# Performance work log

Measured on AMD Instinct MI355X. Metric: run time of the kernel, lower is better.

## Reference

```python
import jax, jax.numpy as jnp
import numpy as np

L, H, C, HS, V, BS = 4, 8, 512, 64, 32000, 2048  # layers, heads, n_embd, head_size, vocab, block_size
B, T = 2, 2048


def _ln(x, g, b, eps=1e-5):
    m = jnp.mean(x, axis=-1, keepdims=True)
    v = jnp.var(x, axis=-1, keepdims=True)
    return (x - m) * jax.lax.rsqrt(v + eps) * g + b


def setup_inputs() -> dict:
    key = jax.random.key(0)
    ks = jax.random.split(key, 12)
    s = 0.02
    f = jnp.float32
    return {
        "idx": jax.random.randint(ks[0], (B, T), 0, V),
        "tok_emb": jax.random.normal(ks[1], (V, C), f) * s,
        "pos_emb": jax.random.normal(ks[2], (BS, C), f) * s,
        "ln1_g": jnp.ones((L, C), f), "ln1_b": jnp.zeros((L, C), f),
        "wq": jax.random.normal(ks[3], (L, H, C, HS), f) * s,
        "wk": jax.random.normal(ks[4], (L, H, C, HS), f) * s,
        "wv": jax.random.normal(ks[5], (L, H, C, HS), f) * s,
        "proj_w": jax.random.normal(ks[6], (L, C, C), f) * s,
        "proj_b": jnp.zeros((L, C), f),
        "ln2_g": jnp.ones((L, C), f), "ln2_b": jnp.zeros((L, C), f),
        "ff_w1": jax.random.normal(ks[7], (L, C, 4 * C), f) * s,
        "ff_b1": jnp.zeros((L, 4 * C), f),
        "ff_w2": jax.random.normal(ks[8], (L, 4 * C, C), f) * s,
        "ff_b2": jnp.zeros((L, C), f),
        "ffln_g": jnp.ones((L, C), f), "ffln_b": jnp.zeros((L, C), f),
        "lm_w": jax.random.normal(ks[9], (C, V), f) * s,
        "lm_b": jnp.zeros((V,), f),
    }


def reference(idx, tok_emb, pos_emb, ln1_g, ln1_b, wq, wk, wv, proj_w, proj_b,
              ln2_g, ln2_b, ff_w1, ff_b1, ff_w2, ff_b2, ffln_g, ffln_b, lm_w, lm_b):
    Tn = idx.shape[1]
    x = tok_emb[idx] + pos_emb[:Tn]  # [B,T,C]
    causal = jnp.tril(jnp.ones((Tn, Tn), bool))
    for l in range(L):
        h = _ln(x, ln1_g[l], ln1_b[l])
        q = jnp.einsum('btc,hcd->bhtd', h, wq[l])
        k = jnp.einsum('btc,hcd->bhtd', h, wk[l])
        v = jnp.einsum('btc,hcd->bhtd', h, wv[l])
        # NOTE: original module does NOT scale by 1/sqrt(head_size)
        wei = jnp.einsum('bhtd,bhsd->bhts', q, k)
        wei = jnp.where(causal, wei, -jnp.inf)
        wei = jax.nn.softmax(wei, axis=-1)
        att = jnp.einsum('bhts,bhsd->bhtd', wei, v)  # [B,H,T,HS]
        att = att.transpose(0, 2, 1, 3).reshape(x.shape[0], Tn, C)
        x = x + att @ proj_w[l].T + proj_b[l]
        h2 = _ln(x, ln2_g[l], ln2_b[l])
        ff = jax.nn.relu(h2 @ ff_w1[l] + ff_b1[l]) @ ff_w2[l] + ff_b2[l]
        ff = _ln(ff, ffln_g[l], ffln_b[l])  # FeedForward has trailing LayerNorm
        x = x + ff
    logits = x @ lm_w + lm_b  # [B,T,V]
    return logits
```

## Files before the change

kernel.cpp:

```cpp
#include <hip/hip_runtime.h>
#include <math.h>

#define NLAYER 4
#define NH     8
#define CDIM   512
#define HS     64
#define VOCAB  32000
#define BB     2
#define TT     2048
#define MROWS  (BB*TT)
#define QKVW   (3*CDIM)
#define NHEADS (BB*NH)

typedef __attribute__((ext_vector_type(8))) short bf16x8;
typedef __attribute__((ext_vector_type(4))) float f32x4;

__device__ __forceinline__ unsigned short f2bf(float f) {
    unsigned int u = __float_as_uint(f);
    u += 0x7FFF + ((u >> 16) & 1);
    return (unsigned short)(u >> 16);
}

#define GLOAD16(g, l) __builtin_amdgcn_global_load_lds( \
    (const __attribute__((address_space(1))) void*)(g), \
    (__attribute__((address_space(3))) void*)(l), 16, 0, 0)

template<int FLAGS, bool OUTBF>
__global__ __launch_bounds__(256) void mfma_gemm(
    const unsigned short* __restrict__ A, int lda,
    const unsigned short* __restrict__ Bt, int ldb,
    const float* __restrict__ bias,
    void* __restrict__ Cout, int ldc,
    const float* __restrict__ resid,
    int K)
{
    __shared__ unsigned short As[128*64];
    __shared__ unsigned short Bs[128*64];
    const int tid = threadIdx.x;
    const int w = tid >> 6, l = tid & 63;
    const int wr = w >> 1, wc = w & 1;
    const long m0 = (long)blockIdx.y * 128;
    const long n0 = (long)blockIdx.x * 128;
    const int srow = l >> 3;
    const int scol = (l & 7) << 3;
    const unsigned short* Ab = A + m0*lda;
    const unsigned short* Bb = Bt + n0*ldb;
    const int fr = l & 15;
    const int fk = (l >> 4) << 3;

    f32x4 acc[4][4];
    #pragma unroll
    for (int m = 0; m < 4; m++)
        #pragma unroll
        for (int n = 0; n < 4; n++) acc[m][n] = (f32x4)0.0f;

    for (int k0 = 0; k0 < K; k0 += 64) {
        __syncthreads();
        #pragma unroll
        for (int i = 0; i < 4; i++) {
            int seg = w*4 + i;
            GLOAD16(Ab + (long)(seg*8 + srow)*lda + k0 + scol, As + seg*512);
            GLOAD16(Bb + (long)(seg*8 + srow)*ldb + k0 + scol, Bs + seg*512);
        }
        __syncthreads();
        #pragma unroll
        for (int kk = 0; kk < 2; kk++) {
            bf16x8 af[4], bf[4];
            #pragma unroll
            for (int m = 0; m < 4; m++)
                af[m] = *(const bf16x8*)&As[(wr*64 + m*16 + fr)*64 + kk*32 + fk];
            #pragma unroll
            for (int n = 0; n < 4; n++)
                bf[n] = *(const bf16x8*)&Bs[(wc*64 + n*16 + fr)*64 + kk*32 + fk];
            #pragma unroll
            for (int m = 0; m < 4; m++)
                #pragma unroll
                for (int n = 0; n < 4; n++)
                    acc[m][n] = __builtin_amdgcn_mfma_f32_16x16x32_bf16(
                        af[m], bf[n], acc[m][n], 0, 0, 0);
        }
    }

    const int rg = (l >> 4) << 2;
    #pragma unroll
    for (int n = 0; n < 4; n++) {
        long gn = n0 + wc*64 + n*16 + fr;
        float bv = (FLAGS & 1) ? bias[gn] : 0.f;
        #pragma unroll
        for (int m = 0; m < 4; m++) {
            #pragma unroll
            for (int r = 0; r < 4; r++) {
                long gm = m0 + wr*64 + m*16 + rg + r;
                float val = acc[m][n][r] + bv;
                if (FLAGS & 2) val = fmaxf(val, 0.f);
                if (FLAGS & 4) val += resid[gm*ldc + gn];
                if (OUTBF) ((unsigned short*)Cout)[gm*ldc + gn] = f2bf(val);
                else       ((float*)Cout)[gm*ldc + gn] = val;
            }
        }
    }
}

__global__ __launch_bounds__(256) void mfma_gemm_qkv(
    const unsigned short* __restrict__ A,
    const unsigned short* __restrict__ Bt,
    unsigned short* __restrict__ qh,
    unsigned short* __restrict__ kh,
    unsigned short* __restrict__ vt)
{
    __shared__ unsigned short As[128*64];
    __shared__ unsigned short Bs[128*64];
    const int tid = threadIdx.x;
    const int w = tid >> 6, l = tid & 63;
    const int wr = w >> 1, wc = w & 1;
    const long m0 = (long)blockIdx.y * 128;
    const long n0 = (long)blockIdx.x * 128;
    const int srow = l >> 3;
    const int scol = (l & 7) << 3;
    const unsigned short* Ab = A + m0*CDIM;
    const unsigned short* Bb = Bt + n0*CDIM;
    const int fr = l & 15;
    const int fk = (l >> 4) << 3;

    f32x4 acc[4][4];
    #pragma unroll
    for (int m = 0; m < 4; m++)
        #pragma unroll
        for (int n = 0; n < 4; n++) acc[m][n] = (f32x4)0.0f;

    for (int k0 = 0; k0 < CDIM; k0 += 64) {
        __syncthreads();
        #pragma unroll
        for (int i = 0; i < 4; i++) {
            int seg = w*4 + i;
            GLOAD16(Ab + (long)(seg*8 + srow)*CDIM + k0 + scol, As + seg*512);
            GLOAD16(Bb + (long)(seg*8 + srow)*CDIM + k0 + scol, Bs + seg*512);
        }
        __syncthreads();
        #pragma unroll
        for (int kk = 0; kk < 2; kk++) {
            bf16x8 af[4], bf[4];
            #pragma unroll
            for (int m = 0; m < 4; m++)
                af[m] = *(const bf16x8*)&As[(wr*64 + m*16 + fr)*64 + kk*32 + fk];
            #pragma unroll
            for (int n = 0; n < 4; n++)
                bf[n] = *(const bf16x8*)&Bs[(wc*64 + n*16 + fr)*64 + kk*32 + fk];
            #pragma unroll
            for (int m = 0; m < 4; m++)
                #pragma unroll
                for (int n = 0; n < 4; n++)
                    acc[m][n] = __builtin_amdgcn_mfma_f32_16x16x32_bf16(
                        af[m], bf[n], acc[m][n], 0, 0, 0);
        }
    }

    const int rg = (l >> 4) << 2;
    #pragma unroll
    for (int n = 0; n < 4; n++) {
        int gn = (int)(n0 + wc*64 + n*16 + fr);
        int which = gn >> 9, hh = (gn >> 6) & 7, d = gn & 63;
        #pragma unroll
        for (int m = 0; m < 4; m++) {
            #pragma unroll
            for (int r = 0; r < 4; r++) {
                int gm = (int)(m0 + wr*64 + m*16 + rg + r);
                int b = gm >> 11, t = gm & (TT-1);
                int head = b*NH + hh;
                unsigned short val = f2bf(acc[m][n][r]);
                if (which == 0)      qh[((long)head*TT + t)*HS + d] = val;
                else if (which == 1) kh[((long)head*TT + t)*HS + d] = val;
                else                 vt[((long)head*HS + d)*TT + t] = val;
            }
        }
    }
}

__global__ __launch_bounds__(256) void attn_part(
    const unsigned short* __restrict__ qh,
    const unsigned short* __restrict__ kh,
    const unsigned short* __restrict__ vt,
    float* __restrict__ oP, float* __restrict__ ml)
{
    __shared__ unsigned short Ks[2][64*64];
    __shared__ unsigned short Vts[2][64*64];
    __shared__ unsigned short Ps[4][32*72];
    const int tid = threadIdx.x;
    const int w = tid >> 6, l = tid & 63;
    const int fr = l & 15, g = l >> 4;
    const int head = blockIdx.y;
    const int sp = blockIdx.z;
    const int x = blockIdx.x;
    const int qt0 = x * 128;
    const int qw = qt0 + w*32;
    const unsigned short* Qb = qh + (long)head*TT*HS;
    const unsigned short* Kb = kh + (long)head*TT*HS;
    const unsigned short* Vb = vt + (long)head*HS*TT;

    bf16x8 aq[2][2];
    #pragma unroll
    for (int mt = 0; mt < 2; mt++)
        #pragma unroll
        for (int ks = 0; ks < 2; ks++)
            aq[mt][ks] = *(const bf16x8*)&Qb[(long)(qw + mt*16 + fr)*HS + ks*32 + g*8];

    f32x4 acc_o[2][4];
    float mrun[2][4], lsum[2][4];
    #pragma unroll
    for (int mt = 0; mt < 2; mt++) {
        #pragma unroll
        for (int r = 0; r < 4; r++) { mrun[mt][r] = -INFINITY; lsum[mt][r] = 0.f; }
        #pragma unroll
        for (int n = 0; n < 4; n++) acc_o[mt][n] = (f32x4)0.0f;
    }

    const int cbeg = sp * (x + 1);
    const int cend = cbeg + (x + 1);
    const int srow = l >> 3;
    const int scol = ((l & 7) ^ (srow & 7)) << 3;

    auto stage = [&](int c) {
        int buf = c & 1;
        int s0_ = c*64;
        #pragma unroll
        for (int i = 0; i < 2; i++) {
            int rb = i*32 + w*8;
            GLOAD16(Kb + (long)(s0_ + rb + srow)*HS + scol, &Ks[buf][rb*64]);
            GLOAD16(Vb + (long)(rb + srow)*TT + s0_ + scol, &Vts[buf][rb*64]);
        }
    };

    stage(cbeg);
    for (int c = cbeg; c < cend; c++) {
        const int s0 = c*64;
        const int buf = c & 1;
        __syncthreads();
        if (c + 1 < cend) stage(c+1);
        if (s0 > qw + 31) continue;

        bf16x8 bk[4][2];
        #pragma unroll
        for (int n = 0; n < 4; n++)
            #pragma unroll
            for (int ks = 0; ks < 2; ks++) {
                int row = n*16 + fr;
                int u = (ks*4 + g) ^ (row & 7);
                bk[n][ks] = *(const bf16x8*)&Ks[buf][row*64 + u*8];
            }
        f32x4 sc[2][4];
        #pragma unroll
        for (int mt = 0; mt < 2; mt++)
            #pragma unroll
            for (int n = 0; n < 4; n++) sc[mt][n] = (f32x4)0.0f;
        #pragma unroll
        for (int ks = 0; ks < 2; ks++)
            #pragma unroll
            for (int mt = 0; mt < 2; mt++)
                #pragma unroll
                for (int n = 0; n < 4; n++)
                    sc[mt][n] = __builtin_amdgcn_mfma_f32_16x16x32_bf16(
                        aq[mt][ks], bk[n][ks], sc[mt][n], 0, 0, 0);

        #pragma unroll
        for (int mt = 0; mt < 2; mt++) {
            #pragma unroll
            for (int r = 0; r < 4; r++) {
                int q = qw + mt*16 + g*4 + r;
                float rmax = -INFINITY;
                #pragma unroll
                for (int n = 0; n < 4; n++) {
                    float v = sc[mt][n][r];
                    v = (s0 + n*16 + fr <= q) ? v : -INFINITY;
                    sc[mt][n][r] = v;
                    rmax = fmaxf(rmax, v);
                }
                #pragma unroll
                for (int off = 8; off >= 1; off >>= 1)
                    rmax = fmaxf(rmax, __shfl_xor(rmax, off));
                float mnew = fmaxf(mrun[mt][r], rmax);
                float scale = __expf(mrun[mt][r] - mnew);
                float ps = 0.f;
                #pragma unroll
                for (int n = 0; n < 4; n++) {
                    float p = __expf(sc[mt][n][r] - mnew);
                    sc[mt][n][r] = p;
                    ps += p;
                }
                #pragma unroll
                for (int off = 8; off >= 1; off >>= 1)
                    ps += __shfl_xor(ps, off);
                lsum[mt][r] = lsum[mt][r]*scale + ps;
                mrun[mt][r] = mnew;
                #pragma unroll
                for (int n = 0; n < 4; n++) acc_o[mt][n][r] *= scale;
            }
        }

        #pragma unroll
        for (int mt = 0; mt < 2; mt++)
            #pragma unroll
            for (int n = 0; n < 4; n++)
                #pragma unroll
                for (int r = 0; r < 4; r++)
                    Ps[w][(mt*16 + g*4 + r)*72 + n*16 + fr] = f2bf(sc[mt][n][r]);

        bf16x8 ap[2][2], bv[4][2];
        #pragma unroll
        for (int mt = 0; mt < 2; mt++)
            #pragma unroll
            for (int ks = 0; ks < 2; ks++)
                ap[mt][ks] = *(const bf16x8*)&Ps[w][(mt*16 + fr)*72 + ks*32 + g*8];
        #pragma unroll
        for (int n = 0; n < 4; n++)
            #pragma unroll
            for (int ks = 0; ks < 2; ks++) {
                int row = n*16 + fr;
                int u = (ks*4 + g) ^ (row & 7);
                bv[n][ks] = *(const bf16x8*)&Vts[buf][row*64 + u*8];
            }
        #pragma unroll
        for (int ks = 0; ks < 2; ks++)
            #pragma unroll
            for (int mt = 0; mt < 2; mt++)
                #pragma unroll
                for (int n = 0; n < 4; n++)
                    acc_o[mt][n] = __builtin_amdgcn_mfma_f32_16x16x32_bf16(
                        ap[mt][ks], bv[n][ks], acc_o[mt][n], 0, 0, 0);
    }

    float* oB = oP + ((long)(head*2 + sp)*TT)*HS;
    float* mlB = ml + ((long)(head*2 + sp)*TT)*2;
    #pragma unroll
    for (int mt = 0; mt < 2; mt++) {
        #pragma unroll
        for (int n = 0; n < 4; n++)
            #pragma unroll
            for (int r = 0; r < 4; r++)
                oB[(long)(qw + mt*16 + g*4 + r)*HS + n*16 + fr] = acc_o[mt][n][r];
        if (fr == 0) {
            #pragma unroll
            for (int r = 0; r < 4; r++) {
                int t = qw + mt*16 + g*4 + r;
                mlB[t*2]     = mrun[mt][r];
                mlB[t*2 + 1] = lsum[mt][r];
            }
        }
    }
}

__global__ __launch_bounds__(256) void attn_combine(
    const float* __restrict__ oP, const float* __restrict__ ml,
    unsigned short* __restrict__ att)
{
    const int gid = blockIdx.x*4 + (threadIdx.x >> 6);
    const int lane = threadIdx.x & 63;
    const int head = gid >> 11, t = gid & (TT-1);
    const int b = head >> 3, hh = head & 7;
    const long i0 = (long)(head*2 + 0)*TT + t;
    const long i1 = (long)(head*2 + 1)*TT + t;
    const float m0 = ml[i0*2], l0 = ml[i0*2+1];
    const float m1 = ml[i1*2], l1 = ml[i1*2+1];
    const float M = fmaxf(m0, m1);
    const float e0 = __expf(m0 - M), e1 = __expf(m1 - M);
    const float L = l0*e0 + l1*e1;
    const float v = (oP[i0*HS + lane]*e0 + oP[i1*HS + lane]*e1) / L;
    att[((long)b*TT + t)*CDIM + hh*HS + lane] = f2bf(v);
}

__global__ __launch_bounds__(256) void transpose_cast(
    const float* __restrict__ in, unsigned short* __restrict__ out,
    int R, int Cn, long in_z1, long in_z2, long out_z1, long out_z2, int z2n)
{
    const int z = blockIdx.z;
    const int z1 = z / z2n, z2 = z % z2n;
    const float* ip = in + (long)z1*in_z1 + (long)z2*in_z2;
    unsigned short* op = out + (long)z1*out_z1 + (long)z2*out_z2;
    __shared__ float tile[32][33];
    const int tx = threadIdx.x & 31, ty = threadIdx.x >> 5;
    const long r0 = (long)blockIdx.y*32, c0 = (long)blockIdx.x*32;
    #pragma unroll
    for (int i = 0; i < 4; i++)
        tile[ty + i*8][tx] = ip[(r0 + ty + i*8)*Cn + c0 + tx];
    __syncthreads();
    #pragma unroll
    for (int i = 0; i < 4; i++)
        op[(c0 + ty + i*8)*R + r0 + tx] = f2bf(tile[tx][ty + i*8]);
}

__global__ __launch_bounds__(256) void cast_kernel(
    const float* __restrict__ in, unsigned short* __restrict__ out, long n)
{
    long i = ((long)blockIdx.x*256 + threadIdx.x) * 4;
    if (i >= n) return;
    float4 v = *(const float4*)(in + i);
    ushort4 u = make_ushort4(f2bf(v.x), f2bf(v.y), f2bf(v.z), f2bf(v.w));
    *(ushort4*)(out + i) = u;
}

__global__ void embed_kernel(const int* __restrict__ idx,
                             const float* __restrict__ tok,
                             const float* __restrict__ pos,
                             float* __restrict__ x)
{
    const int r = blockIdx.x;
    const int t = r & (TT-1);
    const long tr = idx[r];
    const float* te = tok + tr*CDIM;
    const float* pe = pos + (long)t*CDIM;
    float* xo = x + (long)r*CDIM;
    for (int c = threadIdx.x; c < CDIM; c += blockDim.x)
        xo[c] = te[c] + pe[c];
}

template<int MODE>
__global__ __launch_bounds__(256) void ln_kernel(
    const float* __restrict__ in, const float* __restrict__ g,
    const float* __restrict__ bb, void* __restrict__ outp,
    void* __restrict__ outp2)
{
    const int wave = threadIdx.x >> 6;
    const int lane = threadIdx.x & 63;
    const long r = (long)blockIdx.x*4 + wave;
    const float* xr = in + r*CDIM;
    float vals[8];
    float s = 0.f;
    #pragma unroll
    for (int i = 0; i < 8; i++) { vals[i] = xr[lane + i*64]; s += vals[i]; }
    #pragma unroll
    for (int o = 32; o >= 1; o >>= 1) s += __shfl_xor(s, o);
    const float mean = s * (1.f/CDIM);
    float vs = 0.f;
    #pragma unroll
    for (int i = 0; i < 8; i++) { float d = vals[i]-mean; vs += d*d; }
    #pragma unroll
    for (int o = 32; o >= 1; o >>= 1) vs += __shfl_xor(vs, o);
    const float rstd = rsqrtf(vs*(1.f/CDIM) + 1e-5f);
    #pragma unroll
    for (int i = 0; i < 8; i++) {
        int c = lane + i*64;
        float nv = (vals[i]-mean)*rstd*g[c] + bb[c];
        if (MODE == 1) {
            ((unsigned short*)outp)[r*CDIM + c] = f2bf(nv);
        } else {
            float s2 = ((float*)outp)[r*CDIM + c] + nv;
            ((float*)outp)[r*CDIM + c] = s2;
            if (MODE == 3) ((unsigned short*)outp2)[r*CDIM + c] = f2bf(s2);
        }
    }
}

extern "C" void kernel_launch(void* const* d_in, const int* in_sizes, int n_in,
                              void* d_out, int out_size, void* d_ws, size_t ws_size,
                              hipStream_t stream)
{
    const int*   idx   = (const int*)  d_in[0];
    const float* tok   = (const float*)d_in[1];
    const float* pos   = (const float*)d_in[2];
    const float* ln1g  = (const float*)d_in[3];
    const float* ln1b  = (const float*)d_in[4];
    const float* wq    = (const float*)d_in[5];
    const float* wk    = (const float*)d_in[6];
    const float* wv    = (const float*)d_in[7];
    const float* projw = (const float*)d_in[8];
    const float* projb = (const float*)d_in[9];
    const float* ln2g  = (const float*)d_in[10];
    const float* ln2b  = (const float*)d_in[11];
    const float* ffw1  = (const float*)d_in[12];
    const float* ffb1  = (const float*)d_in[13];
    const float* ffw2  = (const float*)d_in[14];
    const float* ffb2  = (const float*)d_in[15];
    const float* flng  = (const float*)d_in[16];
    const float* flnb  = (const float*)d_in[17];
    const float* lmw   = (const float*)d_in[18];
    const float* lmb   = (const float*)d_in[19];
    float* out = (float*)d_out;

    char* wp = (char*)d_ws;
    float* x  = (float*)wp;           wp += (size_t)MROWS*CDIM*4;
    float* ff = (float*)wp;           wp += (size_t)MROWS*CDIM*4;
    unsigned short* h     = (unsigned short*)wp; wp += (size_t)MROWS*CDIM*2;
    unsigned short* lmt   = (unsigned short*)wp; wp += (size_t)VOCAB*CDIM*2;
    unsigned short* ff1t  = (unsigned short*)wp; wp += (size_t)NLAYER*4*CDIM*CDIM*2;
    unsigned short* ff2t  = (unsigned short*)wp; wp += (size_t)NLAYER*4*CDIM*CDIM*2;
    unsigned short* qkvt  = (unsigned short*)wp; wp += (size_t)NLAYER*QKVW*CDIM*2;
    unsigned short* projc = (unsigned short*)wp; wp += (size_t)NLAYER*CDIM*CDIM*2;
    unsigned short* qh    = (unsigned short*)wp; wp += (size_t)NHEADS*TT*HS*2;
    unsigned short* kh    = (unsigned short*)wp; wp += (size_t)NHEADS*TT*HS*2;
    unsigned short* vt    = (unsigned short*)wp; wp += (size_t)NHEADS*TT*HS*2;

    unsigned short* f1  = (unsigned short*)d_out;
    unsigned short* att = f1 + (size_t)MROWS*4*CDIM;
    float* oP = (float*)(att + (size_t)MROWS*CDIM);
    float* ml = oP + (size_t)NHEADS*2*TT*HS;

    transpose_cast<<<dim3(VOCAB/32, CDIM/32, 1), 256, 0, stream>>>(
        lmw, lmt, CDIM, VOCAB, 0, 0, 0, 0, 1);
    transpose_cast<<<dim3(4*CDIM/32, CDIM/32, NLAYER), 256, 0, stream>>>(
        ffw1, ff1t, CDIM, 4*CDIM, (long)CDIM*4*CDIM, 0, (long)4*CDIM*CDIM, 0, 1);
    transpose_cast<<<dim3(CDIM/32, 4*CDIM/32, NLAYER), 256, 0, stream>>>(
        ffw2, ff2t, 4*CDIM, CDIM, (long)4*CDIM*CDIM, 0, (long)CDIM*4*CDIM, 0, 1);
    {
        const size_t QBLK = (size_t)CDIM * CDIM;
        transpose_cast<<<dim3(HS/32, CDIM/32, NLAYER*NH), 256, 0, stream>>>(
            wq, qkvt,            CDIM, HS,
            (long)NH*CDIM*HS, (long)CDIM*HS, (long)QKVW*CDIM, (long)HS*CDIM, NH);
        transpose_cast<<<dim3(HS/32, CDIM/32, NLAYER*NH), 256, 0, stream>>>(
            wk, qkvt + QBLK,     CDIM, HS,
            (long)NH*CDIM*HS, (long)CDIM*HS, (long)QKVW*CDIM, (long)HS*CDIM, NH);
        transpose_cast<<<dim3(HS/32, CDIM/32, NLAYER*NH), 256, 0, stream>>>(
            wv, qkvt + 2*QBLK,   CDIM, HS,
            (long)NH*CDIM*HS, (long)CDIM*HS, (long)QKVW*CDIM, (long)HS*CDIM, NH);
    }
    cast_kernel<<<(NLAYER*CDIM*CDIM/4 + 255)/256, 256, 0, stream>>>(
        projw, projc, (long)NLAYER*CDIM*CDIM);

    embed_kernel<<<MROWS, 256, 0, stream>>>(idx, tok, pos, x);

    for (int l = 0; l < NLAYER; l++) {
        const unsigned short* qkvt_l = qkvt + (size_t)l*QKVW*CDIM;
        const unsigned short* projc_l = projc + (size_t)l*CDIM*CDIM;
        const unsigned short* ff1t_l = ff1t + (size_t)l*4*CDIM*CDIM;
        const unsigned short* ff2t_l = ff2t + (size_t)l*4*CDIM*CDIM;

        ln_kernel<1><<<MROWS/4, 256, 0, stream>>>(x, ln1g + l*CDIM, ln1b + l*CDIM, h, nullptr);

        mfma_gemm_qkv<<<dim3(QKVW/128, MROWS/128), 256, 0, stream>>>(
            h, qkvt_l, qh, kh, vt);

        attn_part<<<dim3(TT/128, NHEADS, 2), 256, 0, stream>>>(qh, kh, vt, oP, ml);
        attn_combine<<<dim3(NHEADS*TT/4), 256, 0, stream>>>(oP, ml, att);

        mfma_gemm<5,false><<<dim3(CDIM/128, MROWS/128), 256, 0, stream>>>(
            att, CDIM, projc_l, CDIM, projb + l*CDIM, x, CDIM, x, CDIM);

        ln_kernel<1><<<MROWS/4, 256, 0, stream>>>(x, ln2g + l*CDIM, ln2b + l*CDIM, h, nullptr);

        mfma_gemm<3,true><<<dim3(4*CDIM/128, MROWS/128), 256, 0, stream>>>(
            h, CDIM, ff1t_l, CDIM, ffb1 + (size_t)l*4*CDIM, f1, 4*CDIM, nullptr, CDIM);

        mfma_gemm<1,false><<<dim3(CDIM/128, MROWS/128), 256, 0, stream>>>(
            f1, 4*CDIM, ff2t_l, 4*CDIM, ffb2 + l*CDIM, ff, CDIM, nullptr, 4*CDIM);

        if (l == NLAYER-1)
            ln_kernel<3><<<MROWS/4, 256, 0, stream>>>(ff, flng + l*CDIM, flnb + l*CDIM, x, h);
        else
            ln_kernel<2><<<MROWS/4, 256, 0, stream>>>(ff, flng + l*CDIM, flnb + l*CDIM, x, nullptr);
    }

    mfma_gemm<1,false><<<dim3(VOCAB/128, MROWS/128), 256, 0, stream>>>(
        h, CDIM, lmt, CDIM, lmb, out, VOCAB, nullptr, CDIM);
}
```

Measured before the change: 1.034 ms.

## Split attention KV four ways with direct global loads; swizzle LM-head GEMM blocks

The attention partial kernel now splits the KV range four ways, interleaving chunks across splits instead of using contiguous halves. It also drops LDS staging of K/V and loads fragments straight from global memory. The causal mask is applied only on the diagonal chunk, and the combine kernel merges four partials. Separately, the LM-head GEMM gets an XCD-aware block swizzle with a transposed grid to improve L2 reuse across chiplets. Risks are uncoalesced global reads replacing the shared-memory path and extra partial-output traffic in the combine step.

```diff
diff --git a/kernel.cpp b/kernel.cpp
--- a/kernel.cpp
+++ b/kernel.cpp
@@ -11,6 +11,7 @@
 #define MROWS  (BB*TT)
 #define QKVW   (3*CDIM)
 #define NHEADS (BB*NH)
+#define NSPLIT 4
 
 typedef __attribute__((ext_vector_type(8))) short bf16x8;
 typedef __attribute__((ext_vector_type(4))) float f32x4;
@@ -25,7 +26,7 @@
     (const __attribute__((address_space(1))) void*)(g), \
     (__attribute__((address_space(3))) void*)(l), 16, 0, 0)
 
-template<int FLAGS, bool OUTBF>
+template<int FLAGS, bool OUTBF, bool MSWIZ>
 __global__ __launch_bounds__(256) void mfma_gemm(
     const unsigned short* __restrict__ A, int lda,
     const unsigned short* __restrict__ Bt, int ldb,
@@ -39,8 +40,18 @@
     const int tid = threadIdx.x;
     const int w = tid >> 6, l = tid & 63;
     const int wr = w >> 1, wc = w & 1;
-    const long m0 = (long)blockIdx.y * 128;
-    const long n0 = (long)blockIdx.x * 128;
+    long m0, n0;
+    if (MSWIZ) {
+        const int mt = gridDim.x;
+        const int flat = blockIdx.y * mt + blockIdx.x;
+        const int cpx = (mt * gridDim.y) >> 3;
+        const int swz = (flat & 7) * cpx + (flat >> 3);
+        m0 = (long)(swz % mt) * 128;
+        n0 = (long)(swz / mt) * 128;
+    } else {
+        m0 = (long)blockIdx.y * 128;
+        n0 = (long)blockIdx.x * 128;
+    }
     const int srow = l >> 3;
     const int scol = (l & 7) << 3;
     const unsigned short* Ab = A + m0*lda;
@@ -182,17 +193,13 @@
     const unsigned short* __restrict__ vt,
     float* __restrict__ oP, float* __restrict__ ml)
 {
-    __shared__ unsigned short Ks[2][64*64];
-    __shared__ unsigned short Vts[2][64*64];
     __shared__ unsigned short Ps[4][32*72];
     const int tid = threadIdx.x;
     const int w = tid >> 6, l = tid & 63;
     const int fr = l & 15, g = l >> 4;
     const int head = blockIdx.y;
     const int sp = blockIdx.z;
-    const int x = blockIdx.x;
-    const int qt0 = x * 128;
-    const int qw = qt0 + w*32;
+    const int qw = (blockIdx.x*4 + w) * 32;
     const unsigned short* Qb = qh + (long)head*TT*HS;
     const unsigned short* Kb = kh + (long)head*TT*HS;
     const unsigned short* Vb = vt + (long)head*HS*TT;
@@ -214,39 +221,17 @@
         for (int n = 0; n < 4; n++) acc_o[mt][n] = (f32x4)0.0f;
     }
 
-    const int cbeg = sp * (x + 1);
-    const int cend = cbeg + (x + 1);
-    const int srow = l >> 3;
-    const int scol = ((l & 7) ^ (srow & 7)) << 3;
-
-    auto stage = [&](int c) {
-        int buf = c & 1;
-        int s0_ = c*64;
-        #pragma unroll
-        for (int i = 0; i < 2; i++) {
-            int rb = i*32 + w*8;
-            GLOAD16(Kb + (long)(s0_ + rb + srow)*HS + scol, &Ks[buf][rb*64]);
-            GLOAD16(Vb + (long)(rb + srow)*TT + s0_ + scol, &Vts[buf][rb*64]);
-        }
-    };
-
-    stage(cbeg);
-    for (int c = cbeg; c < cend; c++) {
+    const int nc = qw/64 + 1;
+    for (int c = sp; c < nc; c += NSPLIT) {
         const int s0 = c*64;
-        const int buf = c & 1;
-        __syncthreads();
-        if (c + 1 < cend) stage(c+1);
-        if (s0 > qw + 31) continue;
 
         bf16x8 bk[4][2];
         #pragma unroll
         for (int n = 0; n < 4; n++)
             #pragma unroll
-            for (int ks = 0; ks < 2; ks++) {
-                int row = n*16 + fr;
-                int u = (ks*4 + g) ^ (row & 7);
-                bk[n][ks] = *(const bf16x8*)&Ks[buf][row*64 + u*8];
-            }
+            for (int ks = 0; ks < 2; ks++)
+                bk[n][ks] = *(const bf16x8*)&Kb[(long)(s0 + n*16 + fr)*HS + ks*32 + g*8];
+
         f32x4 sc[2][4];
         #pragma unroll
         for (int mt = 0; mt < 2; mt++)
@@ -261,19 +246,24 @@
                     sc[mt][n] = __builtin_amdgcn_mfma_f32_16x16x32_bf16(
                         aq[mt][ks], bk[n][ks], sc[mt][n], 0, 0, 0);
 
+        if (c == nc - 1) {
+            #pragma unroll
+            for (int mt = 0; mt < 2; mt++)
+                #pragma unroll
+                for (int r = 0; r < 4; r++) {
+                    int q = qw + mt*16 + g*4 + r;
+                    #pragma unroll
+                    for (int n = 0; n < 4; n++)
+                        if (s0 + n*16 + fr > q) sc[mt][n][r] = -INFINITY;
+                }
+        }
+
         #pragma unroll
         for (int mt = 0; mt < 2; mt++) {
             #pragma unroll
             for (int r = 0; r < 4; r++) {
-                int q = qw + mt*16 + g*4 + r;
-                float rmax = -INFINITY;
-                #pragma unroll
-                for (int n = 0; n < 4; n++) {
-                    float v = sc[mt][n][r];
-                    v = (s0 + n*16 + fr <= q) ? v : -INFINITY;
-                    sc[mt][n][r] = v;
-                    rmax = fmaxf(rmax, v);
-                }
+                float rmax = fmaxf(fmaxf(sc[mt][0][r], sc[mt][1][r]),
+                                   fmaxf(sc[mt][2][r], sc[mt][3][r]));
                 #pragma unroll
                 for (int off = 8; off >= 1; off >>= 1)
                     rmax = fmaxf(rmax, __shfl_xor(rmax, off));
@@ -313,11 +303,8 @@
         #pragma unroll
         for (int n = 0; n < 4; n++)
             #pragma unroll
-            for (int ks = 0; ks < 2; ks++) {
-                int row = n*16 + fr;
-                int u = (ks*4 + g) ^ (row & 7);
-                bv[n][ks] = *(const bf16x8*)&Vts[buf][row*64 + u*8];
-            }
+            for (int ks = 0; ks < 2; ks++)
+                bv[n][ks] = *(const bf16x8*)&Vb[(long)(n*16 + fr)*TT + s0 + ks*32 + g*8];
         #pragma unroll
         for (int ks = 0; ks < 2; ks++)
             #pragma unroll
@@ -328,8 +315,8 @@
                         ap[mt][ks], bv[n][ks], acc_o[mt][n], 0, 0, 0);
     }
 
-    float* oB = oP + ((long)(head*2 + sp)*TT)*HS;
-    float* mlB = ml + ((long)(head*2 + sp)*TT)*2;
+    float* oB = oP + ((long)(head*NSPLIT + sp)*TT)*HS;
+    float* mlB = ml + ((long)(head*NSPLIT + sp)*TT)*2;
     #pragma unroll
     for (int mt = 0; mt < 2; mt++) {
         #pragma unroll
@@ -356,15 +343,22 @@
     const int lane = threadIdx.x & 63;
     const int head = gid >> 11, t = gid & (TT-1);
     const int b = head >> 3, hh = head & 7;
-    const long i0 = (long)(head*2 + 0)*TT + t;
-    const long i1 = (long)(head*2 + 1)*TT + t;
-    const float m0 = ml[i0*2], l0 = ml[i0*2+1];
-    const float m1 = ml[i1*2], l1 = ml[i1*2+1];
-    const float M = fmaxf(m0, m1);
-    const float e0 = __expf(m0 - M), e1 = __expf(m1 - M);
-    const float L = l0*e0 + l1*e1;
-    const float v = (oP[i0*HS + lane]*e0 + oP[i1*HS + lane]*e1) / L;
-    att[((long)b*TT + t)*CDIM + hh*HS + lane] = f2bf(v);
+    float m[NSPLIT], lv[NSPLIT];
+    float M = -INFINITY;
+    #pragma unroll
+    for (int s = 0; s < NSPLIT; s++) {
+        long i = (long)(head*NSPLIT + s)*TT + t;
+        m[s] = ml[i*2]; lv[s] = ml[i*2+1];
+        M = fmaxf(M, m[s]);
+    }
+    float L = 0.f, v = 0.f;
+    #pragma unroll
+    for (int s = 0; s < NSPLIT; s++) {
+        float e = __expf(m[s] - M);
+        L += lv[s]*e;
+        v += oP[((long)(head*NSPLIT + s)*TT + t)*HS + lane]*e;
+    }
+    att[((long)b*TT + t)*CDIM + hh*HS + lane] = f2bf(v / L);
 }
 
 __global__ __launch_bounds__(256) void transpose_cast(
@@ -491,7 +485,7 @@
     unsigned short* f1  = (unsigned short*)d_out;
     unsigned short* att = f1 + (size_t)MROWS*4*CDIM;
     float* oP = (float*)(att + (size_t)MROWS*CDIM);
-    float* ml = oP + (size_t)NHEADS*2*TT*HS;
+    float* ml = oP + (size_t)NHEADS*NSPLIT*TT*HS;
 
     transpose_cast<<<dim3(VOCAB/32, CDIM/32, 1), 256, 0, stream>>>(
         lmw, lmt, CDIM, VOCAB, 0, 0, 0, 0, 1);
@@ -527,18 +521,18 @@
         mfma_gemm_qkv<<<dim3(QKVW/128, MROWS/128), 256, 0, stream>>>(
             h, qkvt_l, qh, kh, vt);
 
-        attn_part<<<dim3(TT/128, NHEADS, 2), 256, 0, stream>>>(qh, kh, vt, oP, ml);
+        attn_part<<<dim3(TT/128, NHEADS, NSPLIT), 256, 0, stream>>>(qh, kh, vt, oP, ml);
         attn_combine<<<dim3(NHEADS*TT/4), 256, 0, stream>>>(oP, ml, att);
 
-        mfma_gemm<5,false><<<dim3(CDIM/128, MROWS/128), 256, 0, stream>>>(
+        mfma_gemm<5,false,false><<<dim3(CDIM/128, MROWS/128), 256, 0, stream>>>(
             att, CDIM, projc_l, CDIM, projb + l*CDIM, x, CDIM, x, CDIM);
 
         ln_kernel<1><<<MROWS/4, 256, 0, stream>>>(x, ln2g + l*CDIM, ln2b + l*CDIM, h, nullptr);
 
-        mfma_gemm<3,true><<<dim3(4*CDIM/128, MROWS/128), 256, 0, stream>>>(
+        mfma_gemm<3,true,false><<<dim3(4*CDIM/128, MROWS/128), 256, 0, stream>>>(
             h, CDIM, ff1t_l, CDIM, ffb1 + (size_t)l*4*CDIM, f1, 4*CDIM, nullptr, CDIM);
 
-        mfma_gemm<1,false><<<dim3(CDIM/128, MROWS/128), 256, 0, stream>>>(
+        mfma_gemm<1,false,false><<<dim3(CDIM/128, MROWS/128), 256, 0, stream>>>(
             f1, 4*CDIM, ff2t_l, 4*CDIM, ffb2 + l*CDIM, ff, CDIM, nullptr, 4*CDIM);
 
         if (l == NLAYER-1)
@@ -547,6 +541,6 @@
             ln_kernel<2><<<MROWS/4, 256, 0, stream>>>(ff, flng + l*CDIM, flnb + l*CDIM, x, nullptr);
     }
 
-    mfma_gemm<1,false><<<dim3(VOCAB/128, MROWS/128), 256, 0, stream>>>(
+    mfma_gemm<1,false,true><<<dim3(MROWS/128, VOCAB/128), 256, 0, stream>>>(
         h, CDIM, lmt, CDIM, lmb, out, VOCAB, nullptr, CDIM);
 }
```

After: 1.131 ms. 1.09x slower.
